# Optimization experiments

Measured on AMD Instinct MI355X. Metric: run time of the kernel, lower is better.

Reference implementation:

```python
import jax, jax.numpy as jnp
import numpy as np

N_NODES = 100000
N_EDGES = 1600000
NUM_FEATURES = 256
HIDDEN_DIM = 128
NUM_CLASSES = 16


def setup_inputs() -> dict:
    key = jax.random.key(0)
    k1, k2, k3, k4 = jax.random.split(key, 4)
    x = jax.random.normal(k1, (N_NODES, NUM_FEATURES), dtype=jnp.float32)
    edge_index = jax.random.randint(k2, (2, N_EDGES), 0, N_NODES, dtype=jnp.int64)
    # Glorot-style init like PyG GCNConv's Linear
    W1 = jax.random.normal(k3, (NUM_FEATURES, HIDDEN_DIM), dtype=jnp.float32) / np.sqrt(NUM_FEATURES)
    b1 = jnp.zeros((HIDDEN_DIM,), dtype=jnp.float32)
    W2 = jax.random.normal(k4, (HIDDEN_DIM, NUM_CLASSES), dtype=jnp.float32) / np.sqrt(HIDDEN_DIM)
    b2 = jnp.zeros((NUM_CLASSES,), dtype=jnp.float32)
    return {"x": x, "edge_index": edge_index, "W1": W1, "b1": b1, "W2": W2, "b2": b2}


def _gcn_norm(edge_index, num_nodes):
    """PyG GCNConv default: add self-loops, symmetric deg^{-1/2} A deg^{-1/2} norm."""
    loops = jnp.arange(num_nodes, dtype=edge_index.dtype)
    row = jnp.concatenate([edge_index[0], loops])  # source
    col = jnp.concatenate([edge_index[1], loops])  # target
    deg = jax.ops.segment_sum(jnp.ones_like(col, dtype=jnp.float32), col,
                              num_segments=num_nodes)
    dinv = jnp.where(deg > 0, jax.lax.rsqrt(deg), 0.0)
    norm = dinv[row] * dinv[col]  # [E + N]
    return row, col, norm


def _gcn_conv(h, row, col, norm, num_nodes):
    # transform first (PyG: lin then propagate), then normalized sum-aggregate
    msg = h[row] * norm[:, None]            # [E+N, d] gather + scale
    return jax.ops.segment_sum(msg, col, num_segments=num_nodes)


def reference(x, edge_index, W1, b1, W2, b2):
    num_nodes = x.shape[0]
    row, col, norm = _gcn_norm(edge_index, num_nodes)
    h = x @ W1
    h = _gcn_conv(h, row, col, norm, num_nodes) + b1
    h = jax.nn.relu(h)
    h = h @ W2
    out = _gcn_conv(h, row, col, norm, num_nodes) + b2
    return out
```

## Files before the change

### kernel.cpp

```cpp
#include <hip/hip_runtime.h>

#define N_NODES 100000
#define N_EDGES 1600000
#define F_IN    256
#define F_HID   128
#define F_OUT   16

#define BSHIFT  9
#define BNODES  512
#define NB      196
#define ECAP    16384
#define CHUNK   4096
#define NCHUNK  ((N_EDGES + CHUNK - 1) / CHUNK)

typedef __attribute__((ext_vector_type(8))) short short8;
typedef __attribute__((ext_vector_type(4))) float float4v;

__device__ __forceinline__ unsigned int bf16_rn(float f) {
    unsigned int u = __float_as_uint(f);
    return (u + 0x7FFFu + ((u >> 16) & 1u)) >> 16;
}
__device__ __forceinline__ unsigned int cvtpk(float lo, float hi) {
    unsigned int r;
    asm("v_cvt_pk_bf16_f32 %0, %1, %2" : "=v"(r) : "v"(lo), "v"(hi));
    return r;
}
__device__ __forceinline__ float blo(unsigned int u) { return __uint_as_float(u << 16); }
__device__ __forceinline__ float bhi(unsigned int u) { return __uint_as_float(u & 0xFFFF0000u); }
__device__ __forceinline__ float bfu(unsigned short u) { return __uint_as_float(((unsigned int)u) << 16); }


__global__ __launch_bounds__(256) void k_binit(int* __restrict__ bcur) {
    int i = threadIdx.x;
    if (i < NB) bcur[i] = i * ECAP;
}

__global__ __launch_bounds__(256) void k_binscatter(const int* __restrict__ rowi,
                                                    const int* __restrict__ coli,
                                                    int* __restrict__ bcur,
                                                    unsigned int* __restrict__ ebuf) {
    __shared__ int cnt[NB], gbase[NB], run[NB];
    int tid = threadIdx.x;
    int e0 = blockIdx.x * CHUNK;
    for (int i = tid; i < NB; i += 256) { cnt[i] = 0; run[i] = 0; }
    __syncthreads();
    int d[16], s[16];
    #pragma unroll
    for (int i = 0; i < 16; i++) {
        int e = e0 + i * 256 + tid;
        if (e < N_EDGES) {
            d[i] = coli[e]; s[i] = rowi[e];
            atomicAdd(&cnt[d[i] >> BSHIFT], 1);
        } else d[i] = -1;
    }
    __syncthreads();
    for (int i = tid; i < NB; i += 256)
        gbase[i] = cnt[i] ? atomicAdd(&bcur[i], cnt[i]) : 0;
    __syncthreads();
    #pragma unroll
    for (int i = 0; i < 16; i++) {
        if (d[i] >= 0) {
            int b = d[i] >> BSHIFT;
            int off = atomicAdd(&run[b], 1);
            ebuf[gbase[b] + off] = ((unsigned int)(d[i] & 511) << 17) | (unsigned int)s[i];
        }
    }
}

__global__ __launch_bounds__(512) void k_finalize(const int* __restrict__ bcur,
                                                  const unsigned int* __restrict__ ebuf,
                                                  int* __restrict__ rp_start,
                                                  int* __restrict__ rp_end,
                                                  float* __restrict__ dinv,
                                                  int* __restrict__ esrc) {
    __shared__ int ndeg[BNODES];
    __shared__ int sc[BNODES];
    int tid = threadIdx.x;
    int b   = blockIdx.x;
    int nb0 = b << BSHIFT;
    int ebeg = b * ECAP, eend = bcur[b];
    ndeg[tid] = 0;
    __syncthreads();
    for (int e = ebeg + tid; e < eend; e += 512)
        atomicAdd(&ndeg[ebuf[e] >> 17], 1);
    __syncthreads();
    sc[tid] = ndeg[tid];
    __syncthreads();
    for (int off = 1; off < BNODES; off <<= 1) {
        int v = (tid >= off) ? sc[tid - off] : 0;
        __syncthreads();
        sc[tid] += v;
        __syncthreads();
    }
    {
        int n = nb0 + tid;
        int deg = ndeg[tid];
        int excl = sc[tid] - deg;
        if (n < N_NODES) {
            rp_start[n] = ebeg + excl;
            rp_end[n]   = ebeg + excl + deg;
            dinv[n]     = rsqrtf(1.0f + (float)deg);
        }
        ndeg[tid] = excl;
    }
    __syncthreads();
    for (int e = ebeg + tid; e < eend; e += 512) {
        unsigned int p = ebuf[e];
        int off = atomicAdd(&ndeg[p >> 17], 1);
        esrc[ebeg + off] = (int)(p & 0x1FFFFu);
    }
}


__global__ __launch_bounds__(256) void k_transW(const float* __restrict__ W1,
                                                ushort* __restrict__ Wt) {
    int t = blockIdx.x * 256 + threadIdx.x;
    int c = t & 127, k = t >> 7;
    Wt[c * 256 + k] = (ushort)cvtpk(W1[k * 128 + c], 0.f);
}


__global__ __launch_bounds__(256) void k_gemm1(const float* __restrict__ x,
                                               const ushort* __restrict__ Wt,
                                               const float* __restrict__ dinv,
                                               ushort* __restrict__ g1) {
    __shared__ ushort Bl[128 * 256];
    const int tid = threadIdx.x;
    const int w = tid >> 6;
    const int l = tid & 63;
    const int m = l & 15;
    const int q = l >> 4;
    const int R0 = blockIdx.x * 128;

    {
        const uint4* Wg = (const uint4*)Wt;
        uint4* Bl4 = (uint4*)Bl;
        #pragma unroll
        for (int it = 0; it < 16; it++) {
            int i = it * 256 + tid;
            int c = i >> 5, j = i & 31;
            Bl4[c * 32 + (j ^ (c & 7))] = Wg[i];
        }
    }
    __syncthreads();

    int r0 = R0 + w * 32 + m;      if (r0 > N_NODES - 1) r0 = N_NODES - 1;
    int r1 = R0 + w * 32 + 16 + m; if (r1 > N_NODES - 1) r1 = N_NODES - 1;
    const float* xr0 = &x[(size_t)r0 * F_IN + q * 8];
    const float* xr1 = &x[(size_t)r1 * F_IN + q * 8];
    const short8* Bl8 = (const short8*)Bl;

    float4v acc[2][8];
    #pragma unroll
    for (int i = 0; i < 2; i++)
        #pragma unroll
        for (int j = 0; j < 8; j++) acc[i][j] = (float4v){0.f, 0.f, 0.f, 0.f};

    #pragma unroll 2
    for (int kt = 0; kt < F_IN; kt += 32) {
        float4 a0 = *(const float4*)&xr0[kt];
        float4 a1 = *(const float4*)&xr0[kt + 4];
        float4 b0 = *(const float4*)&xr1[kt];
        float4 b1 = *(const float4*)&xr1[kt + 4];
        short8 af0, af1;
        ((uint*)&af0)[0] = cvtpk(a0.x, a0.y); ((uint*)&af0)[1] = cvtpk(a0.z, a0.w);
        ((uint*)&af0)[2] = cvtpk(a1.x, a1.y); ((uint*)&af0)[3] = cvtpk(a1.z, a1.w);
        ((uint*)&af1)[0] = cvtpk(b0.x, b0.y); ((uint*)&af1)[1] = cvtpk(b0.z, b0.w);
        ((uint*)&af1)[2] = cvtpk(b1.x, b1.y); ((uint*)&af1)[3] = cvtpk(b1.z, b1.w);
        int jq = (kt >> 3) + q;
        #pragma unroll
        for (int n = 0; n < 8; n++) {
            int col = n * 16 + m;
            short8 bfr = Bl8[col * 32 + (jq ^ (col & 7))];
            acc[0][n] = __builtin_amdgcn_mfma_f32_16x16x32_bf16(af0, bfr, acc[0][n], 0, 0, 0);
            acc[1][n] = __builtin_amdgcn_mfma_f32_16x16x32_bf16(af1, bfr, acc[1][n], 0, 0, 0);
        }
    }

    const int rbase = R0 + w * 32 + q * 4;
    float dv0[4], dv1[4];
    #pragma unroll
    for (int r = 0; r < 4; r++) {
        int v0 = rbase + r;      dv0[r] = (v0 < N_NODES) ? dinv[v0] : 0.f;
        int v1 = rbase + 16 + r; dv1[r] = (v1 < N_NODES) ? dinv[v1] : 0.f;
    }
    #pragma unroll
    for (int n = 0; n < 8; n++) {
        #pragma unroll
        for (int r = 0; r < 4; r++) {
            int v0 = rbase + r;
            if (v0 < N_NODES) {
                float f = dv0[r] * acc[0][n][r];
                g1[v0 * F_HID + n * 16 + m] = (ushort)cvtpk(f, f);
            }
            int v1 = rbase + 16 + r;
            if (v1 < N_NODES) {
                float f = dv1[r] * acc[1][n][r];
                g1[v1 * F_HID + n * 16 + m] = (ushort)cvtpk(f, f);
            }
        }
    }
}


__global__ __launch_bounds__(256) void k_agg1g2(const int* __restrict__ rp_start,
                                                const int* __restrict__ rp_end,
                                                const int* __restrict__ esrc,
                                                const float* __restrict__ dinv,
                                                const unsigned int* __restrict__ g1,
                                                const float* __restrict__ b1,
                                                const float* __restrict__ W2,
                                                ushort* __restrict__ g2b) {
    __shared__ float hl[4][132];
    const int tid  = threadIdx.x;
    const int wave = tid >> 6;
    const int lane = tid & 63;
    const int col  = lane & 15, part = lane >> 4;

    float w2r[32];
    #pragma unroll
    for (int i = 0; i < 32; i++) w2r[i] = W2[i * 64 + lane];

    float2 bb = ((const float2*)b1)[lane];

    #pragma unroll 1
    for (int j = 0; j < 4; j++) {
        const int node = blockIdx.x * 16 + j * 4 + wave;
        int s = rp_start[node], t = rp_end[node];
        unsigned int u = g1[node * 64 + lane];
        float ax = blo(u), ay = bhi(u);
        int e = s;
        for (; e + 7 < t; e += 8) {
            int r0 = esrc[e],     r1 = esrc[e + 1], r2 = esrc[e + 2], r3 = esrc[e + 3];
            int r4 = esrc[e + 4], r5 = esrc[e + 5], r6 = esrc[e + 6], r7 = esrc[e + 7];
            unsigned int u0 = g1[r0 * 64 + lane], u1 = g1[r1 * 64 + lane];
            unsigned int u2 = g1[r2 * 64 + lane], u3 = g1[r3 * 64 + lane];
            unsigned int u4 = g1[r4 * 64 + lane], u5 = g1[r5 * 64 + lane];
            unsigned int u6 = g1[r6 * 64 + lane], u7 = g1[r7 * 64 + lane];
            ax += blo(u0) + blo(u1) + blo(u2) + blo(u3)
                + blo(u4) + blo(u5) + blo(u6) + blo(u7);
            ay += bhi(u0) + bhi(u1) + bhi(u2) + bhi(u3)
                + bhi(u4) + bhi(u5) + bhi(u6) + bhi(u7);
        }
        for (; e + 3 < t; e += 4) {
            int r0 = esrc[e], r1 = esrc[e + 1], r2 = esrc[e + 2], r3 = esrc[e + 3];
            unsigned int u0 = g1[r0 * 64 + lane], u1 = g1[r1 * 64 + lane];
            unsigned int u2 = g1[r2 * 64 + lane], u3 = g1[r3 * 64 + lane];
            ax += blo(u0) + blo(u1) + blo(u2) + blo(u3);
            ay += bhi(u0) + bhi(u1) + bhi(u2) + bhi(u3);
        }
        for (; e < t; e++) {
            unsigned int u0 = g1[esrc[e] * 64 + lane];
            ax += blo(u0); ay += bhi(u0);
        }
        float wv = dinv[node];
        hl[wave][lane * 2]     = fmaxf(fmaf(wv, ax, bb.x), 0.0f);
        hl[wave][lane * 2 + 1] = fmaxf(fmaf(wv, ay, bb.y), 0.0f);

        float acc = 0.f;
        #pragma unroll
        for (int i = 0; i < 32; i++)
            acc = fmaf(hl[wave][i * 4 + part], w2r[i], acc);
        acc += __shfl_xor(acc, 16);
        acc += __shfl_xor(acc, 32);
        if (lane < 16) g2b[node * 16 + col] = (ushort)bf16_rn(wv * acc);
    }
}


__global__ __launch_bounds__(256) void k_agg2(const int* __restrict__ rp_start,
                                              const int* __restrict__ rp_end,
                                              const int* __restrict__ esrc,
                                              const float* __restrict__ dinv,
                                              const ushort* __restrict__ g2b,
                                              const float* __restrict__ b2,
                                              float* __restrict__ out) {
    int gid = blockIdx.x * 256 + threadIdx.x;
    int node = gid >> 4;
    int f = gid & 15;
    if (node >= N_NODES) return;
    int s = rp_start[node], t = rp_end[node];
    float acc = bfu(g2b[node * 16 + f]);
    int e = s;
    for (; e + 7 < t; e += 8) {
        float a0 = bfu(g2b[esrc[e] * 16 + f]),     a1 = bfu(g2b[esrc[e + 1] * 16 + f]);
        float a2 = bfu(g2b[esrc[e + 2] * 16 + f]), a3 = bfu(g2b[esrc[e + 3] * 16 + f]);
        float a4 = bfu(g2b[esrc[e + 4] * 16 + f]), a5 = bfu(g2b[esrc[e + 5] * 16 + f]);
        float a6 = bfu(g2b[esrc[e + 6] * 16 + f]), a7 = bfu(g2b[esrc[e + 7] * 16 + f]);
        acc += a0 + a1 + a2 + a3 + a4 + a5 + a6 + a7;
    }
    for (; e + 3 < t; e += 4) {
        acc += bfu(g2b[esrc[e] * 16 + f]) + bfu(g2b[esrc[e + 1] * 16 + f])
             + bfu(g2b[esrc[e + 2] * 16 + f]) + bfu(g2b[esrc[e + 3] * 16 + f]);
    }
    for (; e < t; e++) acc += bfu(g2b[esrc[e] * 16 + f]);
    out[node * 16 + f] = fmaf(dinv[node], acc, b2[f]);
}


extern "C" void kernel_launch(void* const* d_in, const int* in_sizes, int n_in,
                              void* d_out, int out_size, void* d_ws, size_t ws_size,
                              hipStream_t stream) {
    const float* x   = (const float*)d_in[0];
    const int*   ei  = (const int*)d_in[1];
    const float* W1  = (const float*)d_in[2];
    const float* b1  = (const float*)d_in[3];
    const float* W2  = (const float*)d_in[4];
    const float* b2  = (const float*)d_in[5];
    float* out = (float*)d_out;

    const int* rowi = ei;
    const int* coli = ei + N_EDGES;

    char* ws = (char*)d_ws;
    int*          bcur     = (int*)(ws + 0);
    int*          rp_start = (int*)(ws + 8192);
    int*          rp_end   = (int*)(ws + 524288);
    float*        dinv     = (float*)(ws + 1048576);
    unsigned int* ebuf     = (unsigned int*)(ws + 2097152);
    int*          esrc     = (int*)(ws + 16777216);
    ushort*       Wt       = (ushort*)(ws + 31457280);
    ushort*       g1       = (ushort*)(ws + 33554432);
    ushort*       g2b      = (ushort*)(ws + 62914560);

    k_binit     <<<1, 256, 0, stream>>>(bcur);
    k_binscatter<<<NCHUNK, 256, 0, stream>>>(rowi, coli, bcur, ebuf);
    k_finalize  <<<NB, 512, 0, stream>>>(bcur, ebuf, rp_start, rp_end, dinv, esrc);
    k_transW    <<<128, 256, 0, stream>>>(W1, Wt);

    k_gemm1     <<<(N_NODES + 127) / 128, 256, 0, stream>>>(x, Wt, dinv, g1);
    k_agg1g2    <<<N_NODES / 16, 256, 0, stream>>>(rp_start, rp_end, esrc, dinv,
                                                   (const unsigned int*)g1, b1, W2, g2b);
    k_agg2      <<<(N_NODES * 16 + 255) / 256, 256, 0, stream>>>(rp_start, rp_end, esrc,
                                                                 dinv, g2b, b2, out);
}
```

Before: 321.3 us.

## Merge CSR build kernels into one cooperative kernel with grid syncs

Replaces four preprocessing launches (bin init, bin scatter, finalize, W1 transpose) with a single cooperative kernel that separates the phases with grid-wide syncs. Each chunk block now processes 4096 edges with 512 threads. The aim is to cut kernel launch gaps and tail overheads between the small kernels. In exchange it adds two grid barriers and requires all NCHUNK (391) blocks of 512 threads to be co-resident, which could fail to launch or serialize if occupancy is insufficient.

```diff
diff --git a/kernel.cpp b/kernel.cpp
--- a/kernel.cpp
+++ b/kernel.cpp
@@ -1,4 +1,7 @@
 #include <hip/hip_runtime.h>
+#include <hip/hip_cooperative_groups.h>
+
+namespace cg = cooperative_groups;
 
 #define N_NODES 100000
 #define N_EDGES 1600000
@@ -30,93 +33,92 @@
 __device__ __forceinline__ float bfu(unsigned short u) { return __uint_as_float(((unsigned int)u) << 16); }
 
 
-__global__ __launch_bounds__(256) void k_binit(int* __restrict__ bcur) {
-    int i = threadIdx.x;
-    if (i < NB) bcur[i] = i * ECAP;
-}
-
-__global__ __launch_bounds__(256) void k_binscatter(const int* __restrict__ rowi,
-                                                    const int* __restrict__ coli,
-                                                    int* __restrict__ bcur,
-                                                    unsigned int* __restrict__ ebuf) {
+__global__ __launch_bounds__(512) void k_csr(const int* __restrict__ rowi,
+                                             const int* __restrict__ coli,
+                                             const float* __restrict__ W1,
+                                             int* __restrict__ bcur,
+                                             unsigned int* __restrict__ ebuf,
+                                             int* __restrict__ rp_start,
+                                             int* __restrict__ rp_end,
+                                             float* __restrict__ dinv,
+                                             int* __restrict__ esrc,
+                                             ushort* __restrict__ Wt) {
+    cg::grid_group grid = cg::this_grid();
     __shared__ int cnt[NB], gbase[NB], run[NB];
-    int tid = threadIdx.x;
-    int e0 = blockIdx.x * CHUNK;
-    for (int i = tid; i < NB; i += 256) { cnt[i] = 0; run[i] = 0; }
-    __syncthreads();
-    int d[16], s[16];
-    #pragma unroll
-    for (int i = 0; i < 16; i++) {
-        int e = e0 + i * 256 + tid;
-        if (e < N_EDGES) {
-            d[i] = coli[e]; s[i] = rowi[e];
-            atomicAdd(&cnt[d[i] >> BSHIFT], 1);
-        } else d[i] = -1;
-    }
-    __syncthreads();
-    for (int i = tid; i < NB; i += 256)
-        gbase[i] = cnt[i] ? atomicAdd(&bcur[i], cnt[i]) : 0;
-    __syncthreads();
-    #pragma unroll
-    for (int i = 0; i < 16; i++) {
-        if (d[i] >= 0) {
-            int b = d[i] >> BSHIFT;
-            int off = atomicAdd(&run[b], 1);
-            ebuf[gbase[b] + off] = ((unsigned int)(d[i] & 511) << 17) | (unsigned int)s[i];
-        }
-    }
-}
-
-__global__ __launch_bounds__(512) void k_finalize(const int* __restrict__ bcur,
-                                                  const unsigned int* __restrict__ ebuf,
-                                                  int* __restrict__ rp_start,
-                                                  int* __restrict__ rp_end,
-                                                  float* __restrict__ dinv,
-                                                  int* __restrict__ esrc) {
-    __shared__ int ndeg[BNODES];
-    __shared__ int sc[BNODES];
-    int tid = threadIdx.x;
-    int b   = blockIdx.x;
-    int nb0 = b << BSHIFT;
-    int ebeg = b * ECAP, eend = bcur[b];
-    ndeg[tid] = 0;
-    __syncthreads();
-    for (int e = ebeg + tid; e < eend; e += 512)
-        atomicAdd(&ndeg[ebuf[e] >> 17], 1);
-    __syncthreads();
-    sc[tid] = ndeg[tid];
-    __syncthreads();
-    for (int off = 1; off < BNODES; off <<= 1) {
-        int v = (tid >= off) ? sc[tid - off] : 0;
-        __syncthreads();
-        sc[tid] += v;
-        __syncthreads();
-    }
-    {
-        int n = nb0 + tid;
-        int deg = ndeg[tid];
-        int excl = sc[tid] - deg;
-        if (n < N_NODES) {
-            rp_start[n] = ebeg + excl;
-            rp_end[n]   = ebeg + excl + deg;
-            dinv[n]     = rsqrtf(1.0f + (float)deg);
-        }
-        ndeg[tid] = excl;
-    }
-    __syncthreads();
-    for (int e = ebeg + tid; e < eend; e += 512) {
-        unsigned int p = ebuf[e];
-        int off = atomicAdd(&ndeg[p >> 17], 1);
-        esrc[ebeg + off] = (int)(p & 0x1FFFFu);
-    }
-}
-
-
-__global__ __launch_bounds__(256) void k_transW(const float* __restrict__ W1,
-                                                ushort* __restrict__ Wt) {
-    int t = blockIdx.x * 256 + threadIdx.x;
-    int c = t & 127, k = t >> 7;
-    Wt[c * 256 + k] = (ushort)cvtpk(W1[k * 128 + c], 0.f);
+    __shared__ int ndeg[BNODES], sc[BNODES];
+    const int tid  = threadIdx.x;
+    const int bid  = blockIdx.x;
+    const int gtid = bid * 512 + tid;
+
+    if (gtid < NB) bcur[gtid] = gtid * ECAP;
+    if (gtid < F_IN * F_HID) {
+        int c = gtid & 127, k = gtid >> 7;
+        Wt[c * 256 + k] = (ushort)cvtpk(W1[k * 128 + c], 0.f);
+    }
+    grid.sync();
+
+    if (bid < NCHUNK) {
+        int e0 = bid * CHUNK;
+        for (int i = tid; i < NB; i += 512) { cnt[i] = 0; run[i] = 0; }
+        __syncthreads();
+        int d[8], s[8];
+        #pragma unroll
+        for (int i = 0; i < 8; i++) {
+            int e = e0 + i * 512 + tid;
+            if (e < N_EDGES) {
+                d[i] = coli[e]; s[i] = rowi[e];
+                atomicAdd(&cnt[d[i] >> BSHIFT], 1);
+            } else d[i] = -1;
+        }
+        __syncthreads();
+        for (int i = tid; i < NB; i += 512)
+            gbase[i] = cnt[i] ? atomicAdd(&bcur[i], cnt[i]) : 0;
+        __syncthreads();
+        #pragma unroll
+        for (int i = 0; i < 8; i++) {
+            if (d[i] >= 0) {
+                int b = d[i] >> BSHIFT;
+                int off = atomicAdd(&run[b], 1);
+                ebuf[gbase[b] + off] = ((unsigned int)(d[i] & 511) << 17) | (unsigned int)s[i];
+            }
+        }
+    }
+    grid.sync();
+
+    if (bid < NB) {
+        int nb0 = bid << BSHIFT;
+        int ebeg = bid * ECAP, eend = bcur[bid];
+        ndeg[tid] = 0;
+        __syncthreads();
+        for (int e = ebeg + tid; e < eend; e += 512)
+            atomicAdd(&ndeg[ebuf[e] >> 17], 1);
+        __syncthreads();
+        sc[tid] = ndeg[tid];
+        __syncthreads();
+        for (int off = 1; off < BNODES; off <<= 1) {
+            int v = (tid >= off) ? sc[tid - off] : 0;
+            __syncthreads();
+            sc[tid] += v;
+            __syncthreads();
+        }
+        {
+            int n = nb0 + tid;
+            int deg = ndeg[tid];
+            int excl = sc[tid] - deg;
+            if (n < N_NODES) {
+                rp_start[n] = ebeg + excl;
+                rp_end[n]   = ebeg + excl + deg;
+                dinv[n]     = rsqrtf(1.0f + (float)deg);
+            }
+            ndeg[tid] = excl;
+        }
+        __syncthreads();
+        for (int e = ebeg + tid; e < eend; e += 512) {
+            unsigned int p = ebuf[e];
+            int off = atomicAdd(&ndeg[p >> 17], 1);
+            esrc[ebeg + off] = (int)(p & 0x1FFFFu);
+        }
+    }
 }
 
 
@@ -323,10 +325,14 @@
     ushort*       g1       = (ushort*)(ws + 33554432);
     ushort*       g2b      = (ushort*)(ws + 62914560);
 
-    k_binit     <<<1, 256, 0, stream>>>(bcur);
-    k_binscatter<<<NCHUNK, 256, 0, stream>>>(rowi, coli, bcur, ebuf);
-    k_finalize  <<<NB, 512, 0, stream>>>(bcur, ebuf, rp_start, rp_end, dinv, esrc);
-    k_transW    <<<128, 256, 0, stream>>>(W1, Wt);
+    {
+        void* args[] = { (void*)&rowi, (void*)&coli, (void*)&W1,
+                         (void*)&bcur, (void*)&ebuf,
+                         (void*)&rp_start, (void*)&rp_end,
+                         (void*)&dinv, (void*)&esrc, (void*)&Wt };
+        hipLaunchCooperativeKernel((void*)k_csr, dim3(NCHUNK), dim3(512),
+                                   args, 0, stream);
+    }
 
     k_gemm1     <<<(N_NODES + 127) / 128, 256, 0, stream>>>(x, Wt, dinv, g1);
     k_agg1g2    <<<N_NODES / 16, 256, 0, stream>>>(rp_start, rp_end, esrc, dinv,
```

Measured after the change: 424.2 us. 32.0% more time.
